# Performance work log

Measured on AMD Instinct MI355X. Metric: run time of the kernel, lower is better.

The kernel has to match this reference:

```python
import jax, jax.numpy as jnp
import numpy as np

N, E, XD = 100000, 300000, 32
H, C = 4, 64          # heads, per-head out channels
D = H * C             # 256, node feature width
L = 3                 # num_message_passing
EPS = 1e-5
NEG_SLOPE = 0.2


def setup_inputs() -> dict:
    key = jax.random.key(0)
    ks = jax.random.split(key, 16)
    s = 0.05
    return {
        "x": jax.random.normal(ks[0], (N, XD), jnp.float32),
        "edge_index": jax.random.randint(ks[1], (2, E), 0, N, jnp.int32),
        "edge_type": jax.random.randint(ks[2], (E,), 0, 3, jnp.int32),
        "edge_feat": jax.random.uniform(ks[3], (E,), jnp.float32),
        # pre-encoder Linear(x_dim -> D)
        "W0": jax.random.normal(ks[4], (XD, D), jnp.float32) * s,
        "b0": jnp.zeros((D,), jnp.float32),
        # per-layer GATv2 params, stacked over L layers
        "Wl": jax.random.normal(ks[5], (L, D, D), jnp.float32) * s,
        "bl": jnp.zeros((L, D), jnp.float32),
        "Wr": jax.random.normal(ks[6], (L, D, D), jnp.float32) * s,
        "br": jnp.zeros((L, D), jnp.float32),
        "We": jax.random.normal(ks[7], (L, 4, D), jnp.float32) * s,  # lin_edge (no bias)
        "att": jax.random.normal(ks[8], (L, H, C), jnp.float32) * s,
        "bo": jnp.zeros((L, D), jnp.float32),
        # graph-mode LayerNorm (single module, reused every layer)
        "gamma": jnp.ones((D,), jnp.float32),
        "beta": jnp.zeros((D,), jnp.float32),
    }


def _graph_layernorm(h, gamma, beta):
    # PyG LayerNorm(mode='graph'): normalize over ALL nodes and features of the graph
    mu = jnp.mean(h)
    hc = h - mu
    var = jnp.mean(hc * hc)
    return hc * jax.lax.rsqrt(var + EPS) * gamma + beta


def _gatv2_layer(h, src, dst, eattr, Wl, bl, Wr, br, We, att, bo):
    xl = (h @ Wl + bl).reshape(N, H, C)
    xr = (h @ Wr + br).reshape(N, H, C)
    ea = (eattr @ We).reshape(E, H, C)
    e = jax.nn.leaky_relu(xl[src] + xr[dst] + ea, NEG_SLOPE)   # [E,H,C]
    alpha = jnp.einsum('ehc,hc->eh', e, att)                    # [E,H]
    amax = jax.ops.segment_max(alpha, dst, num_segments=N)     # [N,H]
    ex = jnp.exp(alpha - amax[dst])
    denom = jax.ops.segment_sum(ex, dst, num_segments=N)       # [N,H]
    a = ex / denom[dst]                                         # softmax per dst node
    msg = xl[src] * a[:, :, None]                               # [E,H,C]
    out = jax.ops.segment_sum(msg, dst, num_segments=N)        # [N,H,C]
    return out.reshape(N, D) + bo


def reference(x, edge_index, edge_type, edge_feat,
              W0, b0, Wl, bl, Wr, br, We, att, bo, gamma, beta):
    # edge feature construction: one-hot(type over 3) ++ scalar feature (== torch cat/where path)
    eattr = jnp.concatenate(
        [jax.nn.one_hot(edge_type, 3, dtype=x.dtype), edge_feat[:, None]], axis=-1)  # [E,4]
    src, dst = edge_index[0], edge_index[1]   # messages flow src -> dst
    h = jax.nn.relu(x @ W0 + b0)              # pre_enc (dropout = identity in eval)
    for i in range(L):
        g = _gatv2_layer(h, src, dst, eattr, Wl[i], bl[i], Wr[i], br[i], We[i], att[i], bo[i])
        h = _graph_layernorm(jax.nn.relu(g), gamma, beta)
    return h
```

## Files before the change

kernel.cpp:

```cpp
#include <hip/hip_runtime.h>
#include <hip/hip_bf16.h>

#define NN 100000
#define EE 300000
#define DD 256
#define HH 4
#define CC 64
#define LL 3
#define SCAN_CHUNK 1024

#define BM 64
#define BK 128
#define MPAD 100096

typedef __attribute__((ext_vector_type(8))) short bh8;
typedef __attribute__((ext_vector_type(4))) float f32x4;

__device__ inline float bf2f(unsigned short u) {
    union { float f; unsigned int i; } c; c.i = ((unsigned int)u) << 16; return c.f;
}
__device__ inline unsigned short f2bf(float x) {
    __hip_bfloat16 b = __float2bfloat16(x);
    return *reinterpret_cast<unsigned short*>(&b);
}

__device__ __forceinline__ float qsum2(float x) {
    x += __int_as_float(__builtin_amdgcn_update_dpp(0, __float_as_int(x), 0xB1, 0xF, 0xF, true));
    x += __int_as_float(__builtin_amdgcn_update_dpp(0, __float_as_int(x), 0x4E, 0xF, 0xF, true));
    return x;
}


__global__ __launch_bounds__(256) void k_count(const int* __restrict__ dst, int* __restrict__ deg, int E_) {
    int e = blockIdx.x * 256 + threadIdx.x;
    if (e < E_) atomicAdd(&deg[dst[e]], 1);
}

__global__ __launch_bounds__(256) void k_scan1(const int* __restrict__ deg, int* __restrict__ bsum, int n) {
    int b = blockIdx.x;
    int base = b * SCAN_CHUNK;
    int t = threadIdx.x;
    int s = 0;
    for (int i = t; i < SCAN_CHUNK; i += 256) {
        int idx = base + i;
        if (idx < n) s += deg[idx];
    }
    __shared__ int sdata[256];
    sdata[t] = s;
    __syncthreads();
    for (int off = 128; off > 0; off >>= 1) {
        if (t < off) sdata[t] += sdata[t + off];
        __syncthreads();
    }
    if (t == 0) bsum[b] = sdata[0];
}

__global__ void k_scan2(const int* __restrict__ bsum, int* __restrict__ boff, int nb,
                        int* __restrict__ offsets, int n) {
    if (threadIdx.x == 0 && blockIdx.x == 0) {
        int run = 0;
        for (int i = 0; i < nb; i++) { boff[i] = run; run += bsum[i]; }
        offsets[n] = run;
    }
}

__global__ __launch_bounds__(256) void k_scan3(const int* __restrict__ deg, const int* __restrict__ boff,
                                               int* __restrict__ offsets, int n) {
    int b = blockIdx.x, t = threadIdx.x;
    int base = b * SCAN_CHUNK;
    int i0 = base + t * 4;
    int v[4]; int sum = 0;
    #pragma unroll
    for (int j = 0; j < 4; j++) {
        int idx = i0 + j;
        v[j] = (idx < n) ? deg[idx] : 0;
        sum += v[j];
    }
    __shared__ int sdata[256];
    sdata[t] = sum;
    __syncthreads();
    for (int off = 1; off < 256; off <<= 1) {
        int x = (t >= off) ? sdata[t - off] : 0;
        __syncthreads();
        sdata[t] += x;
        __syncthreads();
    }
    int excl = (t == 0) ? 0 : sdata[t - 1];
    int run = boff[b] + excl;
    #pragma unroll
    for (int j = 0; j < 4; j++) {
        int idx = i0 + j;
        if (idx < n) offsets[idx] = run;
        run += v[j];
    }
}

__global__ __launch_bounds__(256) void k_fill(const int* __restrict__ src, const int* __restrict__ dst,
                                              const int* __restrict__ ety, const float* __restrict__ efe,
                                              const int* __restrict__ offsets, int* __restrict__ cursor,
                                              int* __restrict__ csr_src, float* __restrict__ csr_feat, int E_) {
    int e = blockIdx.x * 256 + threadIdx.x;
    if (e < E_) {
        int d = dst[e];
        int pos = offsets[d] + atomicAdd(&cursor[d], 1);
        csr_src[pos] = src[e] | (ety[e] << 24);
        csr_feat[pos] = efe[e];
    }
}

__global__ __launch_bounds__(256) void k_cvtw(const float* __restrict__ Wl, const float* __restrict__ Wr,
                                              unsigned short* __restrict__ Wct) {
    int mat = blockIdx.z;
    int layer = mat >> 1, which = mat & 1;
    const float* src = (which ? Wr : Wl) + (size_t)layer * DD * DD;
    unsigned short* dst = Wct + (size_t)layer * 512 * DD + (size_t)which * DD * DD;
    int k0 = blockIdx.x * 64, n0 = blockIdx.y * 64;
    __shared__ float tile[64][65];
    int tx = threadIdx.x & 63, ty = threadIdx.x >> 6;
    #pragma unroll
    for (int i = 0; i < 16; i++) {
        int r = i * 4 + ty;
        tile[r][tx] = src[(size_t)(k0 + r) * DD + n0 + tx];
    }
    __syncthreads();
    #pragma unroll
    for (int i = 0; i < 16; i++) {
        int r = i * 4 + ty;
        dst[(size_t)(n0 + r) * DD + k0 + tx] = f2bf(tile[tx][r]);
    }
}

__global__ __launch_bounds__(256) void k_bias(const float* __restrict__ bl, const float* __restrict__ br,
                                              float* __restrict__ bc) {
    int i = blockIdx.x * 256 + threadIdx.x;
    if (i < LL * 512) {
        int l = i >> 9, j = i & 511;
        bc[i] = (j < 256) ? bl[l * DD + j] : br[l * DD + j - 256];
    }
}

__global__ __launch_bounds__(256) void k_preenc(const float* __restrict__ x, const float* __restrict__ W0,
                                                const float* __restrict__ b0, unsigned short* __restrict__ act) {
    __shared__ float xs[8][32];
    int t = threadIdx.x;
    int nb = blockIdx.x * 8;
    {
        int m = t >> 5, k = t & 31;
        xs[m][k] = x[(size_t)(nb + m) * 32 + k];
    }
    __syncthreads();
    float acc[8];
    float b = b0[t];
    #pragma unroll
    for (int m = 0; m < 8; m++) acc[m] = b;
    for (int k = 0; k < 32; k++) {
        float w = W0[k * DD + t];
        #pragma unroll
        for (int m = 0; m < 8; m++) acc[m] += xs[m][k] * w;
    }
    #pragma unroll
    for (int m = 0; m < 8; m++) {
        act[(size_t)(nb + m) * DD + t] = f2bf(fmaxf(acc[m], 0.f));
    }
}

__global__ __launch_bounds__(512) void k_gemm(const unsigned short* __restrict__ act,
                                              const unsigned short* __restrict__ Wct,
                                              const float* __restrict__ bc,
                                              unsigned short* __restrict__ xlr) {
    __shared__ short As[BM][136];
    __shared__ short Bs[512][136];
    short* stage = &Bs[0][0];
    int t = threadIdx.x;
    int lane = t & 63;
    int w = t >> 6;
    size_t rowBase = (size_t)blockIdx.x * BM;
    int rsel = lane & 15, kq = lane >> 4;

    f32x4 acc[4][4];
    #pragma unroll
    for (int i = 0; i < 4; i++)
        #pragma unroll
        for (int j = 0; j < 4; j++)
            acc[i][j] = (f32x4){0.f, 0.f, 0.f, 0.f};

    for (int ks = 0; ks < 2; ++ks) {
        __syncthreads();
        #pragma unroll
        for (int j = 0; j < 2; ++j) {
            int idx = t + j * 512;
            int row = idx >> 4, c16 = idx & 15;
            *(bh8*)&As[row][c16 * 8] =
                *(const bh8*)(act + (rowBase + row) * DD + ks * BK + c16 * 8);
        }
        #pragma unroll
        for (int j = 0; j < 16; ++j) {
            int idx = t + j * 512;
            int row = idx >> 4, c16 = idx & 15;
            *(bh8*)&Bs[row][c16 * 8] =
                *(const bh8*)(Wct + (size_t)row * DD + ks * BK + c16 * 8);
        }
        __syncthreads();
        #pragma unroll
        for (int kk = 0; kk < BK; kk += 32) {
            bh8 af[4], bfr[4];
            int ksel = kk + kq * 8;
            #pragma unroll
            for (int mi = 0; mi < 4; mi++)
                af[mi] = *(const bh8*)&As[mi * 16 + rsel][ksel];
            #pragma unroll
            for (int ni = 0; ni < 4; ni++)
                bfr[ni] = *(const bh8*)&Bs[w * 64 + ni * 16 + rsel][ksel];
            #pragma unroll
            for (int mi = 0; mi < 4; mi++)
                #pragma unroll
                for (int ni = 0; ni < 4; ni++)
                    acc[mi][ni] = __builtin_amdgcn_mfma_f32_16x16x32_bf16(af[mi], bfr[ni], acc[mi][ni], 0, 0, 0);
        }
    }

    __syncthreads();
    #pragma unroll
    for (int ni = 0; ni < 4; ni++) {
        int col = w * 64 + ni * 16 + rsel;
        float bias = bc[col];
        #pragma unroll
        for (int mi = 0; mi < 4; mi++) {
            int r0 = mi * 16 + kq * 4;
            #pragma unroll
            for (int j = 0; j < 4; j++)
                stage[(r0 + j) * 544 + col] = (short)f2bf(acc[mi][ni][j] + bias);
        }
    }
    __syncthreads();
    #pragma unroll
    for (int j = 0; j < 8; ++j) {
        int idx = t + j * 512;
        int row = idx >> 6, c16 = idx & 63;
        size_t grow = rowBase + row;
        if (grow < NN)
            *(bh8*)(xlr + grow * 512 + c16 * 8) = *(const bh8*)&stage[row * 544 + c16 * 8];
    }
}

__global__ __launch_bounds__(256) void k_aggregate(const unsigned short* __restrict__ xlr,
                                                   const int* __restrict__ offsets,
                                                   const int* __restrict__ csr_src, const float* __restrict__ csr_feat,
                                                   const float* __restrict__ We, const float* __restrict__ att,
                                                   const float* __restrict__ bo,
                                                   unsigned short* __restrict__ act, float2* __restrict__ partial) {
    __shared__ __align__(16) float lut[4 * 768];
    int lane = threadIdx.x & 63;
    int wid = threadIdx.x >> 6;
    int n = blockIdx.x * 4 + wid;
    int c0 = lane * 4;
    float* myl = &lut[wid * 768];

    float4 attv = *(const float4*)(att + c0);
    float4 we3 = *(const float4*)(We + 3 * DD + c0);
    float4 w0v = *(const float4*)(We + 0 * DD + c0);
    float4 w1v = *(const float4*)(We + 1 * DD + c0);
    float4 w2v = *(const float4*)(We + 2 * DD + c0);

    uint2 xrr = *(const uint2*)(xlr + (size_t)n * 512 + 256 + c0);
    float xr0 = bf2f((unsigned short)(xrr.x & 0xffff));
    float xr1 = bf2f((unsigned short)(xrr.x >> 16));
    float xr2 = bf2f((unsigned short)(xrr.y & 0xffff));
    float xr3 = bf2f((unsigned short)(xrr.y >> 16));

    *(float4*)&myl[c0]        = make_float4(xr0 + w0v.x, xr1 + w0v.y, xr2 + w0v.z, xr3 + w0v.w);
    *(float4*)&myl[256 + c0]  = make_float4(xr0 + w1v.x, xr1 + w1v.y, xr2 + w1v.z, xr3 + w1v.w);
    *(float4*)&myl[512 + c0]  = make_float4(xr0 + w2v.x, xr1 + w2v.y, xr2 + w2v.z, xr3 + w2v.w);

    int start = offsets[n], end = offsets[n + 1];
    float s = 0.f, a0 = 0.f, a1 = 0.f, a2 = 0.f, a3 = 0.f;
    int i = start;
    for (; i + 2 <= end; i += 2) {
        int pA = csr_src[i];     float fA = csr_feat[i];
        int pB = csr_src[i + 1]; float fB = csr_feat[i + 1];
        uint2 xvA = *(const uint2*)(xlr + (size_t)(pA & 0xFFFFF) * 512 + c0);
        uint2 xvB = *(const uint2*)(xlr + (size_t)(pB & 0xFFFFF) * 512 + c0);
        float4 sA = *(const float4*)&myl[(pA >> 24) * 256 + c0];
        float4 sB = *(const float4*)&myl[(pB >> 24) * 256 + c0];
        float xA0 = bf2f((unsigned short)(xvA.x & 0xffff));
        float xA1 = bf2f((unsigned short)(xvA.x >> 16));
        float xA2 = bf2f((unsigned short)(xvA.y & 0xffff));
        float xA3 = bf2f((unsigned short)(xvA.y >> 16));
        float xB0 = bf2f((unsigned short)(xvB.x & 0xffff));
        float xB1 = bf2f((unsigned short)(xvB.x >> 16));
        float xB2 = bf2f((unsigned short)(xvB.y & 0xffff));
        float xB3 = bf2f((unsigned short)(xvB.y >> 16));
        float eA0 = xA0 + fmaf(fA, we3.x, sA.x); eA0 = fmaxf(eA0, 0.2f * eA0);
        float eA1 = xA1 + fmaf(fA, we3.y, sA.y); eA1 = fmaxf(eA1, 0.2f * eA1);
        float eA2 = xA2 + fmaf(fA, we3.z, sA.z); eA2 = fmaxf(eA2, 0.2f * eA2);
        float eA3 = xA3 + fmaf(fA, we3.w, sA.w); eA3 = fmaxf(eA3, 0.2f * eA3);
        float eB0 = xB0 + fmaf(fB, we3.x, sB.x); eB0 = fmaxf(eB0, 0.2f * eB0);
        float eB1 = xB1 + fmaf(fB, we3.y, sB.y); eB1 = fmaxf(eB1, 0.2f * eB1);
        float eB2 = xB2 + fmaf(fB, we3.z, sB.z); eB2 = fmaxf(eB2, 0.2f * eB2);
        float eB3 = xB3 + fmaf(fB, we3.w, sB.w); eB3 = fmaxf(eB3, 0.2f * eB3);
        float dA = attv.x * eA0 + attv.y * eA1 + attv.z * eA2 + attv.w * eA3;
        float dB = attv.x * eB0 + attv.y * eB1 + attv.z * eB2 + attv.w * eB3;
        dA = qsum2(dA);               dB = qsum2(dB);
        dA += __shfl_xor(dA, 4, 64);  dB += __shfl_xor(dB, 4, 64);
        dA += __shfl_xor(dA, 8, 64);  dB += __shfl_xor(dB, 8, 64);
        float pa = __expf(fminf(fmaxf(dA, -60.f), 60.f));
        float pb = __expf(fminf(fmaxf(dB, -60.f), 60.f));
        s += pa + pb;
        a0 = fmaf(pa, xA0, fmaf(pb, xB0, a0));
        a1 = fmaf(pa, xA1, fmaf(pb, xB1, a1));
        a2 = fmaf(pa, xA2, fmaf(pb, xB2, a2));
        a3 = fmaf(pa, xA3, fmaf(pb, xB3, a3));
    }
    if (i < end) {
        int pA = csr_src[i]; float fA = csr_feat[i];
        uint2 xvA = *(const uint2*)(xlr + (size_t)(pA & 0xFFFFF) * 512 + c0);
        float4 sA = *(const float4*)&myl[(pA >> 24) * 256 + c0];
        float xA0 = bf2f((unsigned short)(xvA.x & 0xffff));
        float xA1 = bf2f((unsigned short)(xvA.x >> 16));
        float xA2 = bf2f((unsigned short)(xvA.y & 0xffff));
        float xA3 = bf2f((unsigned short)(xvA.y >> 16));
        float eA0 = xA0 + fmaf(fA, we3.x, sA.x); eA0 = fmaxf(eA0, 0.2f * eA0);
        float eA1 = xA1 + fmaf(fA, we3.y, sA.y); eA1 = fmaxf(eA1, 0.2f * eA1);
        float eA2 = xA2 + fmaf(fA, we3.z, sA.z); eA2 = fmaxf(eA2, 0.2f * eA2);
        float eA3 = xA3 + fmaf(fA, we3.w, sA.w); eA3 = fmaxf(eA3, 0.2f * eA3);
        float dA = attv.x * eA0 + attv.y * eA1 + attv.z * eA2 + attv.w * eA3;
        dA = qsum2(dA);
        dA += __shfl_xor(dA, 4, 64);
        dA += __shfl_xor(dA, 8, 64);
        float pa = __expf(fminf(fmaxf(dA, -60.f), 60.f));
        s += pa;
        a0 = fmaf(pa, xA0, a0);
        a1 = fmaf(pa, xA1, a1);
        a2 = fmaf(pa, xA2, a2);
        a3 = fmaf(pa, xA3, a3);
    }
    float inv = (end > start) ? __builtin_amdgcn_rcpf(s) : 0.f;
    float4 bov = *(const float4*)(bo + c0);
    float o0 = fmaxf(fmaf(a0, inv, bov.x), 0.f);
    float o1 = fmaxf(fmaf(a1, inv, bov.y), 0.f);
    float o2 = fmaxf(fmaf(a2, inv, bov.z), 0.f);
    float o3 = fmaxf(fmaf(a3, inv, bov.w), 0.f);
    uint2 pk;
    pk.x = (unsigned int)f2bf(o0) | ((unsigned int)f2bf(o1) << 16);
    pk.y = (unsigned int)f2bf(o2) | ((unsigned int)f2bf(o3) << 16);
    *(uint2*)(act + (size_t)n * DD + c0) = pk;

    float v1 = o0 + o1 + o2 + o3;
    float v2 = o0 * o0 + o1 * o1 + o2 * o2 + o3 * o3;
    v1 = qsum2(v1); v2 = qsum2(v2);
    #pragma unroll
    for (int off = 4; off <= 32; off <<= 1) {
        v1 += __shfl_xor(v1, off, 64);
        v2 += __shfl_xor(v2, off, 64);
    }
    if (lane == 0) partial[n] = make_float2(v1, v2);
}

__global__ __launch_bounds__(256) void k_lnreduce(const float2* __restrict__ partial,
                                                  double2* __restrict__ partial2) {
    int b = blockIdx.x, t = threadIdx.x;
    double s1 = 0.0, s2 = 0.0;
    for (int i = b * 256 + t; i < NN; i += 64 * 256) {
        float2 p = partial[i];
        s1 += p.x; s2 += p.y;
    }
    __shared__ double d1[256], d2[256];
    d1[t] = s1; d2[t] = s2;
    __syncthreads();
    for (int off = 128; off > 0; off >>= 1) {
        if (t < off) { d1[t] += d1[t + off]; d2[t] += d2[t + off]; }
        __syncthreads();
    }
    if (t == 0) partial2[b] = (double2){d1[0], d2[0]};
}

__global__ __launch_bounds__(256) void k_stats(const double2* __restrict__ partial2,
                                               const float* __restrict__ gamma, const float* __restrict__ beta,
                                               float* __restrict__ sc, float* __restrict__ vsh) {
    __shared__ double d1[64], d2[64];
    int t = threadIdx.x;
    if (t < 64) { double2 p = partial2[t]; d1[t] = p.x; d2[t] = p.y; }
    __syncthreads();
    for (int off = 32; off > 0; off >>= 1) {
        if (t < off) { d1[t] += d1[t + off]; d2[t] += d2[t + off]; }
        __syncthreads();
    }
    const double M = (double)NN * DD;
    double mu = d1[0] / M;
    double var = d2[0] / M - mu * mu;
    float rs = rsqrtf((float)(var + 1e-5));
    float scv = rs * gamma[t];
    sc[t] = scv;
    vsh[t] = beta[t] - (float)mu * scv;
}

__global__ __launch_bounds__(256) void k_foldw(const unsigned short* __restrict__ Wct,
                                               const float* __restrict__ bcL,
                                               const float* __restrict__ sc, const float* __restrict__ vsh,
                                               unsigned short* __restrict__ Wct2, float* __restrict__ bc2) {
    int row = (blockIdx.x << 2) + (threadIdx.x >> 6);
    int lane = threadIdx.x & 63;
    int k0 = lane * 4;
    uint2 raw = *(const uint2*)(Wct + (size_t)row * DD + k0);
    float w0 = bf2f((unsigned short)(raw.x & 0xffff));
    float w1 = bf2f((unsigned short)(raw.x >> 16));
    float w2 = bf2f((unsigned short)(raw.y & 0xffff));
    float w3 = bf2f((unsigned short)(raw.y >> 16));
    float4 scv = *(const float4*)(sc + k0);
    float4 vv  = *(const float4*)(vsh + k0);
    uint2 pk;
    pk.x = (unsigned int)f2bf(w0 * scv.x) | ((unsigned int)f2bf(w1 * scv.y) << 16);
    pk.y = (unsigned int)f2bf(w2 * scv.z) | ((unsigned int)f2bf(w3 * scv.w) << 16);
    *(uint2*)(Wct2 + (size_t)row * DD + k0) = pk;
    float d = w0 * vv.x + w1 * vv.y + w2 * vv.z + w3 * vv.w;
    #pragma unroll
    for (int off = 32; off > 0; off >>= 1) d += __shfl_xor(d, off, 64);
    if (lane == 0) bc2[row] = bcL[row] + d;
}

__global__ __launch_bounds__(256) void k_final(const unsigned short* __restrict__ act,
                                               const float* __restrict__ sc, const float* __restrict__ vsh,
                                               float* __restrict__ h) {
    size_t i = ((size_t)blockIdx.x * 256 + threadIdx.x) * 4;
    uint2 raw = *(const uint2*)(act + i);
    int ch = (int)(i & (DD - 1));
    float4 scv = *(const float4*)(sc + ch);
    float4 vv  = *(const float4*)(vsh + ch);
    float4 o;
    o.x = fmaf(bf2f((unsigned short)(raw.x & 0xffff)), scv.x, vv.x);
    o.y = fmaf(bf2f((unsigned short)(raw.x >> 16)),    scv.y, vv.y);
    o.z = fmaf(bf2f((unsigned short)(raw.y & 0xffff)), scv.z, vv.z);
    o.w = fmaf(bf2f((unsigned short)(raw.y >> 16)),    scv.w, vv.w);
    *reinterpret_cast<float4*>(h + i) = o;
}


extern "C" void kernel_launch(void* const* d_in, const int* in_sizes, int n_in,
                              void* d_out, int out_size, void* d_ws, size_t ws_size,
                              hipStream_t stream) {
    const float* x    = (const float*)d_in[0];
    const int*   ei   = (const int*)d_in[1];
    const int*   ety  = (const int*)d_in[2];
    const float* efe  = (const float*)d_in[3];
    const float* W0   = (const float*)d_in[4];
    const float* b0   = (const float*)d_in[5];
    const float* Wl   = (const float*)d_in[6];
    const float* bl   = (const float*)d_in[7];
    const float* Wr   = (const float*)d_in[8];
    const float* br   = (const float*)d_in[9];
    const float* We   = (const float*)d_in[10];
    const float* att  = (const float*)d_in[11];
    const float* bo   = (const float*)d_in[12];
    const float* gamma= (const float*)d_in[13];
    const float* beta = (const float*)d_in[14];
    float* h = (float*)d_out;

    char* base = (char*)d_ws;
    size_t off = 0;
    auto carve = [&](size_t bytes) -> void* {
        void* p = base + off;
        off += (bytes + 255) & ~(size_t)255;
        return p;
    };
    unsigned short* act  = (unsigned short*)carve((size_t)MPAD * DD * 2);
    unsigned short* xlr  = (unsigned short*)carve((size_t)NN * 512 * 2);
    unsigned short* Wct  = (unsigned short*)carve((size_t)LL * 512 * DD * 2);
    unsigned short* Wct2 = (unsigned short*)carve((size_t)512 * DD * 2);
    float* bc            = (float*)carve((size_t)LL * 512 * 4);
    float* bc2           = (float*)carve((size_t)512 * 4);
    float* sc            = (float*)carve((size_t)DD * 4);
    float* vsh           = (float*)carve((size_t)DD * 4);
    int*   deg      = (int*)carve((size_t)NN * 4);
    int*   offsets  = (int*)carve((size_t)(NN + 1) * 4);
    int*   bsum     = (int*)carve(1024);
    int*   boff     = (int*)carve(1024);
    int*   csr_src  = (int*)carve((size_t)EE * 4);
    float* csr_feat = (float*)carve((size_t)EE * 4);
    float2* partial = (float2*)carve((size_t)NN * 8);
    double2* partial2 = (double2*)carve((size_t)64 * 16);

    const int NB = (NN + SCAN_CHUNK - 1) / SCAN_CHUNK;

    hipMemsetAsync(deg, 0, (size_t)NN * 4, stream);
    k_count<<<(EE + 255) / 256, 256, 0, stream>>>(ei + EE, deg, EE);
    k_scan1<<<NB, 256, 0, stream>>>(deg, bsum, NN);
    k_scan2<<<1, 64, 0, stream>>>(bsum, boff, NB, offsets, NN);
    k_scan3<<<NB, 256, 0, stream>>>(deg, boff, offsets, NN);
    hipMemsetAsync(deg, 0, (size_t)NN * 4, stream);
    k_fill<<<(EE + 255) / 256, 256, 0, stream>>>(ei, ei + EE, ety, efe, offsets, deg,
                                                 csr_src, csr_feat, EE);

    k_cvtw<<<dim3(4, 4, 6), 256, 0, stream>>>(Wl, Wr, Wct);
    k_bias<<<6, 256, 0, stream>>>(bl, br, bc);

    k_preenc<<<NN / 8, 256, 0, stream>>>(x, W0, b0, act);

    for (int l = 0; l < LL; l++) {
        const unsigned short* Wg = (l == 0) ? Wct : Wct2;
        const float* bg = (l == 0) ? bc : bc2;
        k_gemm<<<MPAD / 64, 512, 0, stream>>>(act, Wg, bg, xlr);
        k_aggregate<<<NN / 4, 256, 0, stream>>>(xlr, offsets, csr_src, csr_feat,
                                                We + (size_t)l * 4 * DD, att + (size_t)l * HH * CC,
                                                bo + (size_t)l * DD, act, partial);
        k_lnreduce<<<64, 256, 0, stream>>>(partial, partial2);
        k_stats<<<1, 256, 0, stream>>>(partial2, gamma, beta, sc, vsh);
        if (l < LL - 1)
            k_foldw<<<128, 256, 0, stream>>>(Wct + (size_t)(l + 1) * 512 * DD, bc + (size_t)(l + 1) * 512,
                                             sc, vsh, Wct2, bc2);
    }
    k_final<<<(NN * DD / 4) / 256, 256, 0, stream>>>(act, sc, vsh, h);
}
```

Baseline: 494.5 us.

## Double-buffer GEMM LDS tiles with register prefetch across four K-steps

Restructures the xl/xr projection GEMM from two K-steps of 128 with synchronous global-to-LDS loads into four K-steps of 64. Tiles are double-buffered in LDS, and the global loads for step k+2 are held in registers while step k's MFMAs run, with one barrier per step. The goal is to hide global load latency behind matrix math. In exchange it uses many more VGPRs for the prefetch registers, which may cut occupancy, and it still allocates about 157KB of LDS per block.

```diff
diff --git a/kernel.cpp b/kernel.cpp
--- a/kernel.cpp
+++ b/kernel.cpp
@@ -10,7 +10,6 @@
 #define SCAN_CHUNK 1024
 
 #define BM 64
-#define BK 128
 #define MPAD 100096
 
 typedef __attribute__((ext_vector_type(8))) short bh8;
@@ -29,6 +28,12 @@
     x += __int_as_float(__builtin_amdgcn_update_dpp(0, __float_as_int(x), 0x4E, 0xF, 0xF, true));
     return x;
 }
+
+#define BARRIER_LGKM() do {                                        \
+    asm volatile("s_waitcnt lgkmcnt(0)" ::: "memory");             \
+    __builtin_amdgcn_s_barrier();                                  \
+    __builtin_amdgcn_sched_barrier(0);                             \
+} while (0)
 
 
 __global__ __launch_bounds__(256) void k_count(const int* __restrict__ dst, int* __restrict__ deg, int E_) {
@@ -168,15 +173,17 @@
                                               const unsigned short* __restrict__ Wct,
                                               const float* __restrict__ bc,
                                               unsigned short* __restrict__ xlr) {
-    __shared__ short As[BM][136];
-    __shared__ short Bs[512][136];
-    short* stage = &Bs[0][0];
+    __shared__ short lds[78336];
     int t = threadIdx.x;
     int lane = t & 63;
     int w = t >> 6;
     size_t rowBase = (size_t)blockIdx.x * BM;
     int rsel = lane & 15, kq = lane >> 4;
 
+    int arow = t >> 3, ac8 = t & 7;
+    const unsigned short* gA = act + (rowBase + arow) * DD + ac8 * 8;
+    int dAo = arow * 68 + ac8 * 8;
+
     f32x4 acc[4][4];
     #pragma unroll
     for (int i = 0; i < 4; i++)
@@ -184,42 +191,68 @@
         for (int j = 0; j < 4; j++)
             acc[i][j] = (f32x4){0.f, 0.f, 0.f, 0.f};
 
-    for (int ks = 0; ks < 2; ++ks) {
-        __syncthreads();
-        #pragma unroll
-        for (int j = 0; j < 2; ++j) {
-            int idx = t + j * 512;
-            int row = idx >> 4, c16 = idx & 15;
-            *(bh8*)&As[row][c16 * 8] =
-                *(const bh8*)(act + (rowBase + row) * DD + ks * BK + c16 * 8);
+    bh8 rB[8], rA;
+    #pragma unroll
+    for (int j = 0; j < 8; ++j) {
+        int idx = t + j * 512; int row = idx >> 3, c8 = idx & 7;
+        rB[j] = *(const bh8*)(Wct + (size_t)row * DD + c8 * 8);
+    }
+    rA = *(const bh8*)(gA);
+    #pragma unroll
+    for (int j = 0; j < 8; ++j) {
+        int idx = t + j * 512; int row = idx >> 3, c8 = idx & 7;
+        *(bh8*)&lds[row * 68 + c8 * 8] = rB[j];
+    }
+    *(bh8*)&lds[69632 + dAo] = rA;
+    #pragma unroll
+    for (int j = 0; j < 8; ++j) {
+        int idx = t + j * 512; int row = idx >> 3, c8 = idx & 7;
+        rB[j] = *(const bh8*)(Wct + (size_t)row * DD + 64 + c8 * 8);
+    }
+    rA = *(const bh8*)(gA + 64);
+    BARRIER_LGKM();
+
+    #pragma unroll
+    for (int ks = 0; ks < 4; ++ks) {
+        const int cur = ks & 1, nxt = cur ^ 1;
+        const int Bc = cur * 34816, Ac = 69632 + cur * 4352;
+        const int Bn = nxt * 34816, An = 69632 + nxt * 4352;
+        if (ks < 3) {
+            #pragma unroll
+            for (int j = 0; j < 8; ++j) {
+                int idx = t + j * 512; int row = idx >> 3, c8 = idx & 7;
+                *(bh8*)&lds[Bn + row * 68 + c8 * 8] = rB[j];
+            }
+            *(bh8*)&lds[An + dAo] = rA;
+        }
+        if (ks < 2) {
+            int ko = (ks + 2) * 64;
+            #pragma unroll
+            for (int j = 0; j < 8; ++j) {
+                int idx = t + j * 512; int row = idx >> 3, c8 = idx & 7;
+                rB[j] = *(const bh8*)(Wct + (size_t)row * DD + ko + c8 * 8);
+            }
+            rA = *(const bh8*)(gA + ko);
         }
         #pragma unroll
-        for (int j = 0; j < 16; ++j) {
-            int idx = t + j * 512;
-            int row = idx >> 4, c16 = idx & 15;
-            *(bh8*)&Bs[row][c16 * 8] =
-                *(const bh8*)(Wct + (size_t)row * DD + ks * BK + c16 * 8);
-        }
-        __syncthreads();
-        #pragma unroll
-        for (int kk = 0; kk < BK; kk += 32) {
+        for (int kk = 0; kk < 64; kk += 32) {
             bh8 af[4], bfr[4];
             int ksel = kk + kq * 8;
             #pragma unroll
             for (int mi = 0; mi < 4; mi++)
-                af[mi] = *(const bh8*)&As[mi * 16 + rsel][ksel];
+                af[mi] = *(const bh8*)&lds[Ac + (mi * 16 + rsel) * 68 + ksel];
             #pragma unroll
             for (int ni = 0; ni < 4; ni++)
-                bfr[ni] = *(const bh8*)&Bs[w * 64 + ni * 16 + rsel][ksel];
+                bfr[ni] = *(const bh8*)&lds[Bc + (w * 64 + ni * 16 + rsel) * 68 + ksel];
             #pragma unroll
             for (int mi = 0; mi < 4; mi++)
                 #pragma unroll
                 for (int ni = 0; ni < 4; ni++)
                     acc[mi][ni] = __builtin_amdgcn_mfma_f32_16x16x32_bf16(af[mi], bfr[ni], acc[mi][ni], 0, 0, 0);
         }
-    }
-
-    __syncthreads();
+        BARRIER_LGKM();
+    }
+
     #pragma unroll
     for (int ni = 0; ni < 4; ni++) {
         int col = w * 64 + ni * 16 + rsel;
@@ -229,7 +262,7 @@
             int r0 = mi * 16 + kq * 4;
             #pragma unroll
             for (int j = 0; j < 4; j++)
-                stage[(r0 + j) * 544 + col] = (short)f2bf(acc[mi][ni][j] + bias);
+                lds[(r0 + j) * 544 + col] = (short)f2bf(acc[mi][ni][j] + bias);
         }
     }
     __syncthreads();
@@ -239,7 +272,7 @@
         int row = idx >> 6, c16 = idx & 63;
         size_t grow = rowBase + row;
         if (grow < NN)
-            *(bh8*)(xlr + grow * 512 + c16 * 8) = *(const bh8*)&stage[row * 544 + c16 * 8];
+            *(bh8*)(xlr + grow * 512 + c16 * 8) = *(const bh8*)&lds[row * 544 + c16 * 8];
     }
 }
 
```

Result: no change. 494.1 us (-0.1%).
